# Performance work log

Measured on AMD Instinct MI355X. Metric: run time of the kernel, lower is better.

The kernel has to match this reference:

```python
import jax, jax.numpy as jnp
import numpy as np

BLOCK = 64
CRIT_TH = 0.5
NEGL_TH = 0.01
TEMP = 1.0
EPS = 1e-6


def setup_inputs() -> dict:
    key = jax.random.key(0)
    kq, kk, kv = jax.random.split(key, 3)
    B, T, H, D = 1, 2048, 8, 64
    q = jax.random.normal(kq, (B, T, H, D), dtype=jnp.float32)
    k = jax.random.normal(kk, (B, T, H, D), dtype=jnp.float32)
    v = jax.random.normal(kv, (B, T, H, D), dtype=jnp.float32)
    return {"q": q, "k": k, "v": v}


def _classify_blocks(qb, kb, D):
    # qb: [B,nq,bs,H,D], kb: [B,nk,bs,H,D]
    q_rep = qb.mean(axis=2)  # [B,nq,H,D]
    k_rep = kb.mean(axis=2)  # [B,nk,H,D]
    bscores = jnp.einsum('bqhd,bkhd->bhqk', q_rep, k_rep) / np.float32(np.sqrt(D))
    ssm = jax.nn.softmax(bscores, axis=-1)
    var = jnp.var(ssm, axis=-1, ddof=1, keepdims=True)  # unbiased, matches torch .var()
    max_scores = bscores.max(axis=-1, keepdims=True)
    imp = var * jnp.maximum(max_scores - bscores.min(), EPS)
    imp_n = (imp - imp.min()) / (imp.max() - imp.min() + EPS)
    crit = imp_n >= CRIT_TH
    negl = imp_n <= NEGL_TH
    marg = (~crit) & (~negl)
    return crit, marg


def reference(q, k, v):
    B, T, H, D = q.shape
    S = k.shape[1]
    nq, nk = T // BLOCK, S // BLOCK  # T,S are multiples of BLOCK (no padding needed)
    dtype = q.dtype

    qb = q.reshape(B, nq, BLOCK, H, D)
    kb = k.reshape(B, nk, BLOCK, H, D)
    vb = v.reshape(B, nk, BLOCK, H, D)

    crit, marg = _classify_blocks(qb, kb, D)  # [B,H,nq,nk] bool
    critf = crit.astype(dtype)
    margf = marg.astype(dtype)

    # ---- exact (critical) blocks: per-block-pair softmax attention ----
    scale = np.float32(1.0 / (np.sqrt(D) * TEMP))
    scores = jnp.einsum('bqthd,bkshd->bhqkts', qb, kb) * scale  # [B,H,nq,nk,bs,bs]
    attn = jax.nn.softmax(scores.astype(jnp.float32), axis=-1).astype(dtype)
    attn_m = attn * critf[:, :, :, :, None, None]
    out_c = jnp.einsum('bhqkts,bkshd->bqthd', attn_m, vb)  # [B,nq,bs,H,D]
    w_c = jnp.einsum('bhqkts->bqth', attn_m)[..., None]    # [B,nq,bs,H,1]

    # ---- linear (marginal) blocks: ELU+1 feature-map attention ----
    qf = jax.nn.elu(qb / TEMP) + 1.0
    kf = jax.nn.elu(kb / TEMP) + 1.0
    kv = jnp.einsum('bkshd,bkshv->bkhdv', kf, vb)              # [B,nk,H,D,D]
    num = jnp.einsum('bqthd,bkhdv->bqkthv', qf, kv)            # [B,nq,nk,bs,H,D]
    k_sum = kf.sum(axis=2)                                     # [B,nk,H,D]
    den = jnp.einsum('bqthd,bkhd->bqkth', qf, k_sum) + EPS     # [B,nq,nk,bs,H]
    out_pair = num / den[..., None]
    out_l = jnp.einsum('bqkthd,bhqk->bqthd', out_pair, margf)
    w_l = jnp.einsum('bqkth,bhqk->bqth', den, margf)[..., None]

    out = (out_c + out_l) / (w_c + w_l + EPS)
    return out.reshape(B, T, H, D)
```

## Files before the change

### kernel.cpp

```cpp
#include <hip/hip_runtime.h>
#include <math.h>

namespace {
constexpr int H  = 8;
constexpr int D  = 64;
constexpr int NB = 32;
constexpr int BS = 64;
constexpr int QST = 68;
}
#define FEPS 1e-6f

typedef unsigned short u16;
typedef unsigned int   u32;
typedef __attribute__((ext_vector_type(8))) short bf16x8;
typedef __attribute__((ext_vector_type(4))) float floatx4;

__device__ __forceinline__ u32 f2bf(float x) {
  union { float f; u32 u; } v; v.f = x;
  return (v.u + 0x7FFFu + ((v.u >> 16) & 1u)) >> 16;
}
__device__ __forceinline__ u32 pk2(float a, float b) { return f2bf(a) | (f2bf(b) << 16); }
#define ELU1(x) ((x) > 0.f ? (x) + 1.f : expf(x))
#define SWZ(row, kblk) ((row)*64 + (((kblk) ^ ((row)&7))*8))

__global__ __launch_bounds__(256) void prep_kernel(const float* __restrict__ q,
                                                   const float* __restrict__ k,
                                                   const float* __restrict__ v,
                                                   u16* __restrict__ kvt16,
                                                   float* __restrict__ ksum,
                                                   double* __restrict__ qrep,
                                                   double* __restrict__ krep) {
  __shared__ float smem[3*BS*D];
  int bid = blockIdx.x;
  int tid = threadIdx.x;
  if (bid >= 256) {
    double* qred = (double*)smem;
    int r = bid - 256;
    int h = r >> 5, bi = r & 31;
    int d = tid & 63, quarter = tid >> 6;
    double s = 0.0;
    for (int t = quarter*16; t < quarter*16 + 16; ++t)
      s += (double)q[((bi*BS + t)*H + h)*D + d];
    qred[quarter*64 + d] = s;
    __syncthreads();
    if (tid < 64)
      qrep[r*D + tid] = (qred[tid] + qred[64+tid] + qred[128+tid] + qred[192+tid]) * (1.0/64.0);
    return;
  }
  float* kf   = smem;
  float* vv   = smem + BS*D;
  float* kraw = smem + 2*BS*D;
  int h = bid >> 5, ki = bid & 31;
  int sr = tid >> 2, cgp = tid & 3;
  const float4* kb = (const float4*)(k + ((ki*BS + sr)*H + h)*D);
  const float4* vb = (const float4*)(v + ((ki*BS + sr)*H + h)*D);
#pragma unroll
  for (int m = 0; m < 4; ++m) {
    float4 kk = kb[cgp*4 + m];
    float4 vx = vb[cgp*4 + m];
    int c = cgp*16 + m*4;
    *(float4*)&kraw[sr*D + c] = kk;
    kf[sr*D + c + 0] = ELU1(kk.x);
    kf[sr*D + c + 1] = ELU1(kk.y);
    kf[sr*D + c + 2] = ELU1(kk.z);
    kf[sr*D + c + 3] = ELU1(kk.w);
    *(float4*)&vv[sr*D + c] = vx;
  }
  __syncthreads();
  int c = tid & 63, dg = tid >> 6, d0 = dg*16;
  float acc[16];
#pragma unroll
  for (int j = 0; j < 16; ++j) acc[j] = 0.f;
#pragma unroll 4
  for (int s2 = 0; s2 < BS; ++s2) {
    float vval = vv[s2*D + c];
    const float4* kr = (const float4*)&kf[s2*D + d0];
    float4 a0 = kr[0], a1 = kr[1], a2 = kr[2], a3 = kr[3];
    acc[0]  += vval*a0.x; acc[1]  += vval*a0.y; acc[2]  += vval*a0.z; acc[3]  += vval*a0.w;
    acc[4]  += vval*a1.x; acc[5]  += vval*a1.y; acc[6]  += vval*a1.z; acc[7]  += vval*a1.w;
    acc[8]  += vval*a2.x; acc[9]  += vval*a2.y; acc[10] += vval*a2.z; acc[11] += vval*a2.w;
    acc[12] += vval*a3.x; acc[13] += vval*a3.y; acc[14] += vval*a3.z; acc[15] += vval*a3.w;
  }
  u16* op = kvt16 + (size_t)bid*4096 + c*64 + d0;
  uint4 P0, P1;
  P0.x = pk2(acc[0],acc[1]);   P0.y = pk2(acc[2],acc[3]);
  P0.z = pk2(acc[4],acc[5]);   P0.w = pk2(acc[6],acc[7]);
  P1.x = pk2(acc[8],acc[9]);   P1.y = pk2(acc[10],acc[11]);
  P1.z = pk2(acc[12],acc[13]); P1.w = pk2(acc[14],acc[15]);
  *(uint4*)(op + 0) = P0;
  *(uint4*)(op + 8) = P1;
  if (dg == 0) {
    float ks = 0.f;
    for (int s2 = 0; s2 < BS; ++s2) ks += kf[s2*D + c];
    ksum[bid*D + c] = ks;
    double m = 0.0;
    for (int s2 = 0; s2 < BS; ++s2) m += (double)kraw[s2*D + c];
    krep[bid*D + c] = m * (1.0/64.0);
  }
}

__global__ __launch_bounds__(256) void bscore_stats_kernel(const double* __restrict__ qrep,
                                                           const double* __restrict__ krep,
                                                           double* __restrict__ rowmin,
                                                           double* __restrict__ rowmax,
                                                           double* __restrict__ rowvar) {
  __shared__ double qs[8*64];
  __shared__ double ks[32*65];
  int b = blockIdx.x;
  int h = b >> 2;
  int r0 = b*8;
  int tid = threadIdx.x;
  for (int i = tid; i < 512; i += 256) qs[i] = qrep[(size_t)r0*64 + i];
  for (int i = tid; i < 2048; i += 256) ks[(i >> 6)*65 + (i & 63)] = krep[(size_t)h*2048 + i];
  __syncthreads();
  int lr = tid >> 5, ki = tid & 31;
  double s = 0.0;
  const double* qr = qs + lr*64;
  const double* kr = ks + ki*65;
#pragma unroll 16
  for (int d = 0; d < D; ++d) s += qr[d]*kr[d];
  double bs = s * 0.125;
  double rmax = bs, rmin = bs;
#pragma unroll
  for (int m = 1; m < 32; m <<= 1) {
    rmax = fmax(rmax, __shfl_xor(rmax, m, 64));
    rmin = fmin(rmin, __shfl_xor(rmin, m, 64));
  }
  double e = exp(bs - rmax);
  double S = e, S2 = e*e;
#pragma unroll
  for (int m = 1; m < 32; m <<= 1) {
    S  += __shfl_xor(S,  m, 64);
    S2 += __shfl_xor(S2, m, 64);
  }
  if (ki == 0) {
    double invS = 1.0 / S;
    double sp = S * invS;
    double mu = sp * (1.0/32.0);
    double var = (S2*invS*invS - 2.0*mu*sp + 32.0*mu*mu) * (1.0/31.0);
    rowmin[r0 + lr] = rmin;
    rowmax[r0 + lr] = rmax;
    rowvar[r0 + lr] = var;
  }
}

__global__ __launch_bounds__(256) void main_kernel(
    const float* __restrict__ q, const float* __restrict__ k, const float* __restrict__ v,
    const u16* __restrict__ kvt16, const float* __restrict__ ksum,
    const double* __restrict__ rowmin, const double* __restrict__ rowmax,
    const double* __restrict__ rowvar, float* __restrict__ out) {
  __shared__ __align__(16) float smem[10304];
  int bid = blockIdx.x;
  int h = bid >> 5, qi = bid & 31;
  int tid = threadIdx.x;
  int row = tid >> 2, cgp = tid & 3, c0 = cgp*16;
  int lane = tid & 63;

  int flag;
  {
    double* buf  = (double*)smem;
    double* impL = (double*)(smem + 512);
    buf[tid] = rowmin[tid];
    __syncthreads();
    for (int s = 128; s > 0; s >>= 1) { if (tid < s) buf[tid] = fmin(buf[tid], buf[tid+s]); __syncthreads(); }
    double gmin = buf[0];
    __syncthreads();
    double rng = rowmax[tid] - gmin;
    if (rng < 1e-6) rng = 1e-6;
    double imp = rowvar[tid] * rng;
    impL[tid] = imp;
    buf[tid] = imp;
    __syncthreads();
    for (int s = 128; s > 0; s >>= 1) { if (tid < s) buf[tid] = fmin(buf[tid], buf[tid+s]); __syncthreads(); }
    double imin = buf[0];
    __syncthreads();
    buf[tid] = imp;
    __syncthreads();
    for (int s = 128; s > 0; s >>= 1) { if (tid < s) buf[tid] = fmax(buf[tid], buf[tid+s]); __syncthreads(); }
    double imax = buf[0];
    __syncthreads();
    double impn = (impL[bid] - imin) / (imax - imin + 1e-6);
    flag = (impn >= 0.5) ? 2 : ((impn <= 0.01) ? 0 : 1);
  }
  __syncthreads();

  if (flag == 1) {
    u16*  qfb  = (u16*)smem;
    u16*  kvb  = (u16*)(smem + 2048);
    float* idens = smem + 6144;
    float* wsl   = smem + 8192;
    float* kslc  = smem + 8256;

    {
      const float4* kss = (const float4*)(ksum + (size_t)(h*NB)*D);
      for (int i = tid; i < NB*16; i += 256) ((float4*)kslc)[i] = kss[i];
    }
    float qf[16];
    {
      const float4* qp = (const float4*)(q + ((qi*BS + row)*H + h)*D + c0);
      float4 q0 = qp[0], q1 = qp[1], q2 = qp[2], q3 = qp[3];
      qf[0]=ELU1(q0.x); qf[1]=ELU1(q0.y); qf[2]=ELU1(q0.z); qf[3]=ELU1(q0.w);
      qf[4]=ELU1(q1.x); qf[5]=ELU1(q1.y); qf[6]=ELU1(q1.z); qf[7]=ELU1(q1.w);
      qf[8]=ELU1(q2.x); qf[9]=ELU1(q2.y); qf[10]=ELU1(q2.z); qf[11]=ELU1(q2.w);
      qf[12]=ELU1(q3.x); qf[13]=ELU1(q3.y); qf[14]=ELU1(q3.z); qf[15]=ELU1(q3.w);
      uint4 p0, p1;
      p0.x = pk2(qf[0],qf[1]);  p0.y = pk2(qf[2],qf[3]);
      p0.z = pk2(qf[4],qf[5]);  p0.w = pk2(qf[6],qf[7]);
      p1.x = pk2(qf[8],qf[9]);  p1.y = pk2(qf[10],qf[11]);
      p1.z = pk2(qf[12],qf[13]); p1.w = pk2(qf[14],qf[15]);
      *(uint4*)&qfb[SWZ(row, cgp*2)]     = p0;
      *(uint4*)&qfb[SWZ(row, cgp*2 + 1)] = p1;
    }
    const u16* kvbase = kvt16 + (size_t)(h*NB)*4096 + row*64 + c0;
    uint4 u0, u1;
    u0 = *(const uint4*)(kvbase + 0);
    u1 = *(const uint4*)(kvbase + 8);
    __syncthreads();
    {
      float wloc = 0.f;
      for (int ki = 0; ki < NB; ++ki) {
        float pd = 0.f;
#pragma unroll
        for (int j = 0; j < 16; ++j) pd += qf[j] * kslc[ki*64 + c0 + j];
        pd += __shfl_xor(pd, 1, 64);
        pd += __shfl_xor(pd, 2, 64);
        float den = pd + FEPS;
        if (cgp == 0) idens[row*32 + ki] = 1.0f / den;
        wloc += den;
      }
      if (cgp == 0) wsl[row] = wloc;
    }
    *(uint4*)&kvb[SWZ(row, cgp*2)]     = u0;
    *(uint4*)&kvb[SWZ(row, cgp*2 + 1)] = u1;

    int w = tid >> 6, m = lane & 15, quad = lane >> 4;
    bf16x8 aLo = *(const bf16x8*)&qfb[SWZ(w*16 + m, quad)];
    bf16x8 aHi = *(const bf16x8*)&qfb[SWZ(w*16 + m, 4 + quad)];
    int rbase = w*16 + quad*4;
    float acc[16];
#pragma unroll
    for (int j = 0; j < 16; ++j) acc[j] = 0.f;

    for (int ki = 0; ki < NB; ++ki) {
      if (ki + 1 < NB) {
        const u16* kvp = kvbase + (size_t)(ki+1)*4096;
        u0 = *(const uint4*)(kvp + 0);
        u1 = *(const uint4*)(kvp + 8);
      }
      __syncthreads();
      const u16* kb = kvb + (ki & 1)*4096;
      float i0 = idens[(rbase + 0)*32 + ki];
      float i1 = idens[(rbase + 1)*32 + ki];
      float i2 = idens[(rbase + 2)*32 + ki];
      float i3 = idens[(rbase + 3)*32 + ki];
      floatx4 zz = {0.f, 0.f, 0.f, 0.f};
#pragma unroll
      for (int t = 0; t < 4; ++t) {
        bf16x8 bLo = *(const bf16x8*)&kb[SWZ(t*16 + m, quad)];
        bf16x8 bHi = *(const bf16x8*)&kb[SWZ(t*16 + m, 4 + quad)];
        floatx4 c4 = __builtin_amdgcn_mfma_f32_16x16x32_bf16(aLo, bLo, zz, 0, 0, 0);
        c4 = __builtin_amdgcn_mfma_f32_16x16x32_bf16(aHi, bHi, c4, 0, 0, 0);
        acc[t*4+0] += c4[0]*i0;
        acc[t*4+1] += c4[1]*i1;
        acc[t*4+2] += c4[2]*i2;
        acc[t*4+3] += c4[3]*i3;
      }
      if (ki + 1 < NB) {
        u16* kw = kvb + ((ki+1) & 1)*4096;
        *(uint4*)&kw[SWZ(row, cgp*2)]     = u0;
        *(uint4*)&kw[SWZ(row, cgp*2 + 1)] = u1;
      }
    }
#pragma unroll
    for (int r = 0; r < 4; ++r) {
      float wd = 1.0f / (wsl[rbase + r] + FEPS);
      float* op = out + ((qi*BS + rbase + r)*H + h)*D + m;
#pragma unroll
      for (int t = 0; t < 4; ++t) op[t*16] = acc[t*4+r]*wd;
    }
    return;
  }

  float* bufA = smem;
  float* bufB = smem + 4352;
  float acc[16];
#pragma unroll
  for (int j = 0; j < 16; ++j) acc[j] = 0.f;
  float wsum = 0.f;

  if (flag == 2) {
    const float4* qp = (const float4*)(q + ((qi*BS + row)*H + h)*D);
#pragma unroll
    for (int mm = 0; mm < 4; ++mm) {
      float4 qq = qp[cgp*4 + mm];
      int c = c0 + mm*4;
      bufA[row*QST + c + 0] = qq.x*0.125f;
      bufA[row*QST + c + 1] = qq.y*0.125f;
      bufA[row*QST + c + 2] = qq.z*0.125f;
      bufA[row*QST + c + 3] = qq.w*0.125f;
    }
    __syncthreads();
    for (int ki = 0; ki < NB; ++ki) {
      const float4* kp = (const float4*)(k + ((ki*BS + row)*H + h)*D);
#pragma unroll
      for (int mm = 0; mm < 4; ++mm)
        *(float4*)&bufB[row*QST + c0 + mm*4] = kp[cgp*4 + mm];
      __syncthreads();
      float sc[16];
#pragma unroll
      for (int j = 0; j < 16; ++j) sc[j] = 0.f;
      for (int d = 0; d < D; ++d) {
        float a = bufA[row*QST + d];
#pragma unroll
        for (int j = 0; j < 16; ++j)
          sc[j] += a * bufB[(c0 + j)*QST + d];
      }
      float mx = sc[0];
#pragma unroll
      for (int j = 1; j < 16; ++j) mx = fmaxf(mx, sc[j]);
      mx = fmaxf(mx, __shfl_xor(mx, 1, 64));
      mx = fmaxf(mx, __shfl_xor(mx, 2, 64));
      float es = 0.f;
      float p[16];
#pragma unroll
      for (int j = 0; j < 16; ++j) { p[j] = expf(sc[j] - mx); es += p[j]; }
      es += __shfl_xor(es, 1, 64);
      es += __shfl_xor(es, 2, 64);
      float inv = 1.0f / es;
#pragma unroll
      for (int j = 0; j < 16; ++j) p[j] *= inv;
      wsum += es * inv;
      __syncthreads();
      const float4* vp = (const float4*)(v + ((ki*BS + row)*H + h)*D);
#pragma unroll
      for (int mm = 0; mm < 4; ++mm)
        *(float4*)&bufB[row*QST + c0 + mm*4] = vp[cgp*4 + mm];
      __syncthreads();
      for (int s2 = 0; s2 < BS; ++s2) {
        int g = s2 >> 4, jj = s2 & 15;
        float pv = __shfl(p[jj], (lane & ~3) | g, 64);
        const float4* vr = (const float4*)&bufB[s2*QST + c0];
        float4 a0 = vr[0], a1 = vr[1], a2 = vr[2], a3 = vr[3];
        acc[0]  += pv*a0.x; acc[1]  += pv*a0.y; acc[2]  += pv*a0.z; acc[3]  += pv*a0.w;
        acc[4]  += pv*a1.x; acc[5]  += pv*a1.y; acc[6]  += pv*a1.z; acc[7]  += pv*a1.w;
        acc[8]  += pv*a2.x; acc[9]  += pv*a2.y; acc[10] += pv*a2.z; acc[11] += pv*a2.w;
        acc[12] += pv*a3.x; acc[13] += pv*a3.y; acc[14] += pv*a3.z; acc[15] += pv*a3.w;
      }
      __syncthreads();
    }
  }
  float wd = 1.0f / (wsum + FEPS);
  float* op = out + ((qi*BS + row)*H + h)*D + c0;
  *(float4*)(op + 0)  = make_float4(acc[0]*wd,  acc[1]*wd,  acc[2]*wd,  acc[3]*wd);
  *(float4*)(op + 4)  = make_float4(acc[4]*wd,  acc[5]*wd,  acc[6]*wd,  acc[7]*wd);
  *(float4*)(op + 8)  = make_float4(acc[8]*wd,  acc[9]*wd,  acc[10]*wd, acc[11]*wd);
  *(float4*)(op + 12) = make_float4(acc[12]*wd, acc[13]*wd, acc[14]*wd, acc[15]*wd);
}

extern "C" void kernel_launch(void* const* d_in, const int* in_sizes, int n_in,
                              void* d_out, int out_size, void* d_ws, size_t ws_size,
                              hipStream_t stream) {
  const float* q = (const float*)d_in[0];
  const float* k = (const float*)d_in[1];
  const float* v = (const float*)d_in[2];
  float* out = (float*)d_out;
  char* ws = (char*)d_ws;
  u16*    kvw  = (u16*)   (ws + 0);
  float*  ksw  = (float*) (ws + 2097152);
  double* krep = (double*)(ws + 2162688);
  double* qrep = (double*)(ws + 2293760);
  double* rmn  = (double*)(ws + 2424832);
  double* rmx  = (double*)(ws + 2426880);
  double* rvr  = (double*)(ws + 2428928);

  prep_kernel<<<512, 256, 0, stream>>>(q, k, v, kvw, ksw, qrep, krep);
  bscore_stats_kernel<<<32, 256, 0, stream>>>(qrep, krep, rmn, rmx, rvr);
  main_kernel<<<256, 256, 0, stream>>>(q, k, v, kvw, ksw, rmn, rmx, rvr, out);
}
```

Baseline: 97.55 us.

## Hoist linear-path loads above classification and stage four KV blocks per sync

Moves the ksum, q feature-map and first KV-block loads ahead of the block classification so their global latency overlaps the reductions. The classification's shared-memory tree reductions become wavefront shuffle reductions with a four-entry cross-wave combine, which removes many barriers. The marginal path now stages four KV blocks in LDS per round, cutting barriers per KV block from one to about half. In exchange, all blocks (including critical ones) issue these loads even when unused, LDS grows to about 60KB, and register use rises, which can reduce occupancy.

```diff
diff --git a/kernel.cpp b/kernel.cpp
--- a/kernel.cpp
+++ b/kernel.cpp
@@ -149,79 +149,95 @@
     const u16* __restrict__ kvt16, const float* __restrict__ ksum,
     const double* __restrict__ rowmin, const double* __restrict__ rowmax,
     const double* __restrict__ rowvar, float* __restrict__ out) {
-  __shared__ __align__(16) float smem[10304];
+  __shared__ __align__(16) float smem[15488];
   int bid = blockIdx.x;
   int h = bid >> 5, qi = bid & 31;
   int tid = threadIdx.x;
   int row = tid >> 2, cgp = tid & 3, c0 = cgp*16;
   int lane = tid & 63;
+  int wid = tid >> 6;
+
+  float* idens = smem + 1024;
+  float* wsl   = smem + 3072;
+  float* kslc  = smem + 3200;
+  u16*   qfb   = (u16*)(smem + 5248);
+  u16*   kvS   = (u16*)(smem + 7296);
+
+  {
+    const float4* kss = (const float4*)(ksum + (size_t)(h*NB)*D);
+    for (int i = tid; i < NB*16; i += 256) ((float4*)kslc)[i] = kss[i];
+  }
+  float qf[16];
+  {
+    const float4* qp = (const float4*)(q + ((qi*BS + row)*H + h)*D + c0);
+    float4 q0 = qp[0], q1 = qp[1], q2 = qp[2], q3 = qp[3];
+    qf[0]=ELU1(q0.x); qf[1]=ELU1(q0.y); qf[2]=ELU1(q0.z); qf[3]=ELU1(q0.w);
+    qf[4]=ELU1(q1.x); qf[5]=ELU1(q1.y); qf[6]=ELU1(q1.z); qf[7]=ELU1(q1.w);
+    qf[8]=ELU1(q2.x); qf[9]=ELU1(q2.y); qf[10]=ELU1(q2.z); qf[11]=ELU1(q2.w);
+    qf[12]=ELU1(q3.x); qf[13]=ELU1(q3.y); qf[14]=ELU1(q3.z); qf[15]=ELU1(q3.w);
+    uint4 p0, p1;
+    p0.x = pk2(qf[0],qf[1]);  p0.y = pk2(qf[2],qf[3]);
+    p0.z = pk2(qf[4],qf[5]);  p0.w = pk2(qf[6],qf[7]);
+    p1.x = pk2(qf[8],qf[9]);  p1.y = pk2(qf[10],qf[11]);
+    p1.z = pk2(qf[12],qf[13]); p1.w = pk2(qf[14],qf[15]);
+    *(uint4*)&qfb[SWZ(row, cgp*2)]     = p0;
+    *(uint4*)&qfb[SWZ(row, cgp*2 + 1)] = p1;
+  }
+  const u16* kvbase = kvt16 + (size_t)(h*NB)*4096 + (size_t)row*64 + c0;
+  uint4 pu0[4], pu1[4];
+#pragma unroll
+  for (int t = 0; t < 4; ++t) {
+    const u16* p = kvbase + (size_t)t*4096;
+    pu0[t] = *(const uint4*)(p);
+    pu1[t] = *(const uint4*)(p + 8);
+  }
 
   int flag;
   {
-    double* buf  = (double*)smem;
-    double* impL = (double*)(smem + 512);
-    buf[tid] = rowmin[tid];
-    __syncthreads();
-    for (int s = 128; s > 0; s >>= 1) { if (tid < s) buf[tid] = fmin(buf[tid], buf[tid+s]); __syncthreads(); }
-    double gmin = buf[0];
-    __syncthreads();
+    double* redA = (double*)smem;
+    double* redB = (double*)(smem + 8);
+    double* impS = (double*)(smem + 16);
+    double x = rowmin[tid];
+#pragma unroll
+    for (int m = 1; m < 64; m <<= 1) x = fmin(x, __shfl_xor(x, m, 64));
+    if (lane == 0) redA[wid] = x;
+    __syncthreads();
+    double gmin = fmin(fmin(redA[0], redA[1]), fmin(redA[2], redA[3]));
     double rng = rowmax[tid] - gmin;
     if (rng < 1e-6) rng = 1e-6;
     double imp = rowvar[tid] * rng;
-    impL[tid] = imp;
-    buf[tid] = imp;
-    __syncthreads();
-    for (int s = 128; s > 0; s >>= 1) { if (tid < s) buf[tid] = fmin(buf[tid], buf[tid+s]); __syncthreads(); }
-    double imin = buf[0];
-    __syncthreads();
-    buf[tid] = imp;
-    __syncthreads();
-    for (int s = 128; s > 0; s >>= 1) { if (tid < s) buf[tid] = fmax(buf[tid], buf[tid+s]); __syncthreads(); }
-    double imax = buf[0];
-    __syncthreads();
-    double impn = (impL[bid] - imin) / (imax - imin + 1e-6);
+    __syncthreads();
+    if (tid == bid) impS[0] = imp;
+    double a = imp, b2 = imp;
+#pragma unroll
+    for (int m = 1; m < 64; m <<= 1) {
+      a  = fmin(a,  __shfl_xor(a,  m, 64));
+      b2 = fmax(b2, __shfl_xor(b2, m, 64));
+    }
+    if (lane == 0) { redA[wid] = a; redB[wid] = b2; }
+    __syncthreads();
+    double imin = fmin(fmin(redA[0], redA[1]), fmin(redA[2], redA[3]));
+    double imax = fmax(fmax(redB[0], redB[1]), fmax(redB[2], redB[3]));
+    double impn = (impS[0] - imin) / (imax - imin + 1e-6);
     flag = (impn >= 0.5) ? 2 : ((impn <= 0.01) ? 0 : 1);
-  }
-  __syncthreads();
+    __syncthreads();
+  }
 
   if (flag == 1) {
-    u16*  qfb  = (u16*)smem;
-    u16*  kvb  = (u16*)(smem + 2048);
-    float* idens = smem + 6144;
-    float* wsl   = smem + 8192;
-    float* kslc  = smem + 8256;
-
-    {
-      const float4* kss = (const float4*)(ksum + (size_t)(h*NB)*D);
-      for (int i = tid; i < NB*16; i += 256) ((float4*)kslc)[i] = kss[i];
-    }
-    float qf[16];
-    {
-      const float4* qp = (const float4*)(q + ((qi*BS + row)*H + h)*D + c0);
-      float4 q0 = qp[0], q1 = qp[1], q2 = qp[2], q3 = qp[3];
-      qf[0]=ELU1(q0.x); qf[1]=ELU1(q0.y); qf[2]=ELU1(q0.z); qf[3]=ELU1(q0.w);
-      qf[4]=ELU1(q1.x); qf[5]=ELU1(q1.y); qf[6]=ELU1(q1.z); qf[7]=ELU1(q1.w);
-      qf[8]=ELU1(q2.x); qf[9]=ELU1(q2.y); qf[10]=ELU1(q2.z); qf[11]=ELU1(q2.w);
-      qf[12]=ELU1(q3.x); qf[13]=ELU1(q3.y); qf[14]=ELU1(q3.z); qf[15]=ELU1(q3.w);
-      uint4 p0, p1;
-      p0.x = pk2(qf[0],qf[1]);  p0.y = pk2(qf[2],qf[3]);
-      p0.z = pk2(qf[4],qf[5]);  p0.w = pk2(qf[6],qf[7]);
-      p1.x = pk2(qf[8],qf[9]);  p1.y = pk2(qf[10],qf[11]);
-      p1.z = pk2(qf[12],qf[13]); p1.w = pk2(qf[14],qf[15]);
-      *(uint4*)&qfb[SWZ(row, cgp*2)]     = p0;
-      *(uint4*)&qfb[SWZ(row, cgp*2 + 1)] = p1;
-    }
-    const u16* kvbase = kvt16 + (size_t)(h*NB)*4096 + row*64 + c0;
-    uint4 u0, u1;
-    u0 = *(const uint4*)(kvbase + 0);
-    u1 = *(const uint4*)(kvbase + 8);
-    __syncthreads();
+    int w = tid >> 6, m = lane & 15, quad = lane >> 4;
+    bf16x8 aLo = *(const bf16x8*)&qfb[SWZ(w*16 + m, quad)];
+    bf16x8 aHi = *(const bf16x8*)&qfb[SWZ(w*16 + m, 4 + quad)];
+    int rbase = w*16 + quad*4;
+
     {
       float wloc = 0.f;
       for (int ki = 0; ki < NB; ++ki) {
-        float pd = 0.f;
-#pragma unroll
-        for (int j = 0; j < 16; ++j) pd += qf[j] * kslc[ki*64 + c0 + j];
+        const float4* ks4 = (const float4*)&kslc[ki*64 + c0];
+        float4 k0 = ks4[0], k1 = ks4[1], k2 = ks4[2], k3 = ks4[3];
+        float pd = qf[0]*k0.x + qf[1]*k0.y + qf[2]*k0.z + qf[3]*k0.w
+                 + qf[4]*k1.x + qf[5]*k1.y + qf[6]*k1.z + qf[7]*k1.w
+                 + qf[8]*k2.x + qf[9]*k2.y + qf[10]*k2.z + qf[11]*k2.w
+                 + qf[12]*k3.x + qf[13]*k3.y + qf[14]*k3.z + qf[15]*k3.w;
         pd += __shfl_xor(pd, 1, 64);
         pd += __shfl_xor(pd, 2, 64);
         float den = pd + FEPS;
@@ -230,46 +246,57 @@
       }
       if (cgp == 0) wsl[row] = wloc;
     }
-    *(uint4*)&kvb[SWZ(row, cgp*2)]     = u0;
-    *(uint4*)&kvb[SWZ(row, cgp*2 + 1)] = u1;
-
-    int w = tid >> 6, m = lane & 15, quad = lane >> 4;
-    bf16x8 aLo = *(const bf16x8*)&qfb[SWZ(w*16 + m, quad)];
-    bf16x8 aHi = *(const bf16x8*)&qfb[SWZ(w*16 + m, 4 + quad)];
-    int rbase = w*16 + quad*4;
+#pragma unroll
+    for (int t = 0; t < 4; ++t) {
+      *(uint4*)&kvS[t*4096 + SWZ(row, cgp*2)]     = pu0[t];
+      *(uint4*)&kvS[t*4096 + SWZ(row, cgp*2 + 1)] = pu1[t];
+    }
+    __syncthreads();
+
     float acc[16];
 #pragma unroll
     for (int j = 0; j < 16; ++j) acc[j] = 0.f;
 
-    for (int ki = 0; ki < NB; ++ki) {
-      if (ki + 1 < NB) {
-        const u16* kvp = kvbase + (size_t)(ki+1)*4096;
-        u0 = *(const uint4*)(kvp + 0);
-        u1 = *(const uint4*)(kvp + 8);
-      }
-      __syncthreads();
-      const u16* kb = kvb + (ki & 1)*4096;
-      float i0 = idens[(rbase + 0)*32 + ki];
-      float i1 = idens[(rbase + 1)*32 + ki];
-      float i2 = idens[(rbase + 2)*32 + ki];
-      float i3 = idens[(rbase + 3)*32 + ki];
-      floatx4 zz = {0.f, 0.f, 0.f, 0.f};
-#pragma unroll
-      for (int t = 0; t < 4; ++t) {
-        bf16x8 bLo = *(const bf16x8*)&kb[SWZ(t*16 + m, quad)];
-        bf16x8 bHi = *(const bf16x8*)&kb[SWZ(t*16 + m, 4 + quad)];
-        floatx4 c4 = __builtin_amdgcn_mfma_f32_16x16x32_bf16(aLo, bLo, zz, 0, 0, 0);
-        c4 = __builtin_amdgcn_mfma_f32_16x16x32_bf16(aHi, bHi, c4, 0, 0, 0);
-        acc[t*4+0] += c4[0]*i0;
-        acc[t*4+1] += c4[1]*i1;
-        acc[t*4+2] += c4[2]*i2;
-        acc[t*4+3] += c4[3]*i3;
-      }
-      if (ki + 1 < NB) {
-        u16* kw = kvb + ((ki+1) & 1)*4096;
-        *(uint4*)&kw[SWZ(row, cgp*2)]     = u0;
-        *(uint4*)&kw[SWZ(row, cgp*2 + 1)] = u1;
-      }
+    for (int rd = 0; rd < 8; ++rd) {
+      uint4 nu0[4], nu1[4];
+      if (rd < 7) {
+#pragma unroll
+        for (int t = 0; t < 4; ++t) {
+          const u16* p = kvbase + (size_t)((rd+1)*4 + t)*4096;
+          nu0[t] = *(const uint4*)(p);
+          nu1[t] = *(const uint4*)(p + 8);
+        }
+      }
+#pragma unroll
+      for (int kk = 0; kk < 4; ++kk) {
+        int ki = rd*4 + kk;
+        const u16* kb = kvS + kk*4096;
+        float i0 = idens[(rbase + 0)*32 + ki];
+        float i1 = idens[(rbase + 1)*32 + ki];
+        float i2 = idens[(rbase + 2)*32 + ki];
+        float i3 = idens[(rbase + 3)*32 + ki];
+        floatx4 zz = {0.f, 0.f, 0.f, 0.f};
+#pragma unroll
+        for (int t = 0; t < 4; ++t) {
+          bf16x8 bLo = *(const bf16x8*)&kb[SWZ(t*16 + m, quad)];
+          bf16x8 bHi = *(const bf16x8*)&kb[SWZ(t*16 + m, 4 + quad)];
+          floatx4 c4 = __builtin_amdgcn_mfma_f32_16x16x32_bf16(aLo, bLo, zz, 0, 0, 0);
+          c4 = __builtin_amdgcn_mfma_f32_16x16x32_bf16(aHi, bHi, c4, 0, 0, 0);
+          acc[t*4+0] += c4[0]*i0;
+          acc[t*4+1] += c4[1]*i1;
+          acc[t*4+2] += c4[2]*i2;
+          acc[t*4+3] += c4[3]*i3;
+        }
+      }
+      __syncthreads();
+      if (rd < 7) {
+#pragma unroll
+        for (int t = 0; t < 4; ++t) {
+          *(uint4*)&kvS[t*4096 + SWZ(row, cgp*2)]     = nu0[t];
+          *(uint4*)&kvS[t*4096 + SWZ(row, cgp*2 + 1)] = nu1[t];
+        }
+      }
+      __syncthreads();
     }
 #pragma unroll
     for (int r = 0; r < 4; ++r) {
```

Result: slower. 120.8 us (+23.8%).
